# Performance work log

Measured on AMD Instinct MI355X. Metric: run time of the kernel, lower is better.

The kernel has to match this reference:

```python
import jax, jax.numpy as jnp
import numpy as np

N_NODES = 10000
N_EDGES = 640000
IN_FEATS = 128
HIDDEN = 128
N_CLASSES = 64
EPS = 0.0


def _linear_params(key, fan_in, fan_out):
    k1, k2 = jax.random.split(key)
    bound = 1.0 / np.sqrt(fan_in)
    W = jax.random.uniform(k1, (fan_in, fan_out), jnp.float32, -bound, bound)
    b = jax.random.uniform(k2, (fan_out,), jnp.float32, -bound, bound)
    return W, b


def setup_inputs() -> dict:
    key = jax.random.key(0)
    ks = jax.random.split(key, 8)
    features = jax.random.normal(ks[0], (N_NODES, IN_FEATS), jnp.float32)
    src = jax.random.randint(ks[1], (N_EDGES,), 0, N_NODES, jnp.int64 if jax.config.jax_enable_x64 else jnp.int32)
    dst = jax.random.randint(ks[2], (N_EDGES,), 0, N_NODES, jnp.int64 if jax.config.jax_enable_x64 else jnp.int32)
    W1, b1 = _linear_params(ks[3], IN_FEATS, HIDDEN)
    W3, b3 = _linear_params(ks[4], HIDDEN, HIDDEN)
    W4, b4 = _linear_params(ks[5], HIDDEN, HIDDEN)
    W2, b2 = _linear_params(ks[6], HIDDEN, N_CLASSES)
    return {"features": features, "src": src, "dst": dst,
            "W1": W1, "b1": b1, "W3": W3, "b3": b3,
            "W4": W4, "b4": b4, "W2": W2, "b2": b2}


def gin_conv(h, src, dst, W, b):
    # sum-aggregate neighbor features: agg[v] = sum_{(u->v)} h[u]
    agg = jax.ops.segment_sum(h[src], dst, num_segments=N_NODES)
    z = (1.0 + EPS) * h + agg
    return z @ W + b


def reference(features, src, dst, W1, b1, W3, b3, W4, b4, W2, b2):
    h = gin_conv(features, src, dst, W1, b1)
    h = jax.nn.relu(h)
    h = gin_conv(h, src, dst, W3, b3)
    h = jax.nn.relu(h)
    h = gin_conv(h, src, dst, W4, b4)
    h = jax.nn.relu(h)
    h = gin_conv(h, src, dst, W2, b2)
    return h
```

## Files before the change

kernel.cpp:

```cpp
#include <hip/hip_runtime.h>
#include <hip/hip_bf16.h>

#define N_NODES 10000
#define N_EDGES 640000
#define FEATS   128
#define CAP     192
#define NBUCK   157
#define ECHUNK  2048
#define NPB     313
#define OSTR    160
#define TILE    8

typedef __attribute__((ext_vector_type(2))) float f32x2;

__device__ __forceinline__ float bflo(uint p) { return __uint_as_float(p << 16); }
__device__ __forceinline__ float bfhi(uint p) { return __uint_as_float(p & 0xffff0000u); }
__device__ __forceinline__ f32x2 unpk(uint p) {
    f32x2 v;
    v.x = __uint_as_float(p << 16);
    v.y = __uint_as_float(p & 0xffff0000u);
    return v;
}


__global__ __launch_bounds__(256) void bin_pack(const int* __restrict__ src,
                                                const int* __restrict__ dst,
                                                uint* __restrict__ bucketed,
                                                ushort* __restrict__ goffs,
                                                const float* __restrict__ features,
                                                ushort* __restrict__ hb0) {
    __shared__ int hist[NBUCK];
    __shared__ int offs[NBUCK + 1];
    __shared__ int scan[256];
    __shared__ uint staging[ECHUNK];
    const int tid = threadIdx.x;
    const int b = blockIdx.x;
    const int e0 = b * ECHUNK;
    for (int i = tid; i < NBUCK; i += 256) hist[i] = 0;
    __syncthreads();
    int dreg[8];
#pragma unroll
    for (int i = 0; i < 8; ++i) {
        int e = e0 + tid + i * 256;
        dreg[i] = (e < N_EDGES) ? dst[e] : -1;
        if (dreg[i] >= 0) atomicAdd(&hist[dreg[i] >> 6], 1);
    }
    __syncthreads();
    int val = (tid < NBUCK) ? hist[tid] : 0;
    scan[tid] = val;
    __syncthreads();
    for (int off = 1; off < 256; off <<= 1) {
        int t = (tid >= off) ? scan[tid - off] : 0;
        __syncthreads();
        scan[tid] += t;
        __syncthreads();
    }
    if (tid < NBUCK) offs[tid] = scan[tid] - val;
    if (tid == 0) offs[NBUCK] = scan[NBUCK - 1];
    for (int i = tid; i < NBUCK; i += 256) hist[i] = 0;
    __syncthreads();
    if (tid <= NBUCK) goffs[b * OSTR + tid] = (ushort)offs[tid];
#pragma unroll
    for (int i = 0; i < 8; ++i) {
        int e = e0 + tid + i * 256;
        if (dreg[i] >= 0) {
            int s = src[e];
            int bk = dreg[i] >> 6;
            int slot = offs[bk] + atomicAdd(&hist[bk], 1);
            staging[slot] = ((uint)s << 6) | (uint)(dreg[i] & 63);
        }
    }
    __syncthreads();
    uint4* gu = (uint4*)(bucketed + (size_t)b * ECHUNK);
    const uint4* lu = (const uint4*)staging;
#pragma unroll
    for (int i = 0; i < ECHUNK / 4 / 256; ++i)
        gu[tid + i * 256] = lu[tid + i * 256];

    const int n4 = N_NODES * FEATS / 4;
    for (int i = b * 256 + tid; i < n4; i += NPB * 256) {
        float4 f = ((const float4*)features)[i];
        __hip_bfloat16 b0 = __float2bfloat16(f.x);
        __hip_bfloat16 b1 = __float2bfloat16(f.y);
        __hip_bfloat16 b2 = __float2bfloat16(f.z);
        __hip_bfloat16 b3 = __float2bfloat16(f.w);
        ushort4 o;
        o.x = *(const ushort*)&b0; o.y = *(const ushort*)&b1;
        o.z = *(const ushort*)&b2; o.w = *(const ushort*)&b3;
        ((ushort4*)hb0)[i] = o;
    }
}


__global__ __launch_bounds__(256) void build_ell(const uint* __restrict__ bucketed,
                                                 const ushort* __restrict__ goffs,
                                                 ushort* __restrict__ ell,
                                                 int* __restrict__ cnts) {
    __shared__ ushort lell[64 * CAP];
    __shared__ int lcur[64];
    const int tid = threadIdx.x;
    const int bk = blockIdx.x;
    if (tid < 64) lcur[tid] = 0;
    __syncthreads();
    for (int b = tid; b < NPB; b += 256) {
        int off0 = goffs[b * OSTR + bk];
        int off1 = goffs[b * OSTR + bk + 1];
        const uint* p0 = bucketed + (size_t)b * ECHUNK;
        for (int i = off0; i < off1; ++i) {
            uint p = p0[i];
            int v = p & 63;
            int slot = atomicAdd(&lcur[v], 1);
            if (slot < CAP) lell[v * CAP + slot] = (ushort)(p >> 6);
        }
    }
    __syncthreads();
    const int node0 = bk * 64;
    int nn = N_NODES - node0;
    if (nn > 64) nn = 64;
    const uint4* lu = (const uint4*)lell;
    uint4* gu = (uint4*)(ell + (size_t)node0 * CAP);
    const int nq = nn * (CAP / 8);
    for (int i = tid; i < nq; i += 256) gu[i] = lu[i];
    for (int v = tid; v < nn; v += 256) {
        int c = lcur[v];
        cnts[node0 + v] = (c > CAP) ? CAP : c;
    }
}


__device__ __forceinline__ void gather_tile(const uint4* __restrict__ hbq,
                                            const int* __restrict__ cnts,
                                            const ushort* __restrict__ ell,
                                            int tile0, int tid,
                                            float (*sZ)[132]) {
    const int lane = tid & 63;
    const int wv = tid >> 6;
    const int g = lane >> 4;
    const int q = lane & 15;
#pragma unroll
    for (int n = 0; n < 2; ++n) {
        const int v = tile0 + wv * 2 + n;
        int cnt = cnts[v];
        if (cnt > CAP) cnt = CAP;
        const ushort* __restrict__ row = ell + (size_t)v * CAP;
        f32x2 acc[4];
#pragma unroll
        for (int i = 0; i < 4; ++i) acc[i] = (f32x2){0.f, 0.f};
        const int jmain = cnt & ~3;
#pragma unroll 2
        for (int j = 0; j < jmain; j += 4) {
            uint2 iv = *(const uint2*)(row + j);
            uint word = (g & 2) ? iv.y : iv.x;
            uint u = (g & 1) ? (word >> 16) : (word & 0xffffu);
            uint4 p = hbq[u * 16 + q];
            acc[0] += unpk(p.x);
            acc[1] += unpk(p.y);
            acc[2] += unpk(p.z);
            acc[3] += unpk(p.w);
        }
        if (jmain < cnt) {
            uint2 iv = *(const uint2*)(row + jmain);
            uint word = (g & 2) ? iv.y : iv.x;
            uint u = (g & 1) ? (word >> 16) : (word & 0xffffu);
            float scale = (jmain + g < cnt) ? 1.0f : 0.0f;
            if (u > N_NODES - 1) u = N_NODES - 1;
            f32x2 s2 = {scale, scale};
            uint4 p = hbq[u * 16 + q];
            acc[0] += unpk(p.x) * s2;
            acc[1] += unpk(p.y) * s2;
            acc[2] += unpk(p.z) * s2;
            acc[3] += unpk(p.w) * s2;
        }
        float a[8] = {acc[0].x, acc[0].y, acc[1].x, acc[1].y,
                      acc[2].x, acc[2].y, acc[3].x, acc[3].y};
#pragma unroll
        for (int d = 16; d < 64; d <<= 1) {
#pragma unroll
            for (int i = 0; i < 8; ++i) a[i] += __shfl_xor(a[i], d);
        }
        if (g == 0) {
            uint4 p = hbq[(size_t)v * 16 + q];
            a[0] += bflo(p.x); a[1] += bfhi(p.x);
            a[2] += bflo(p.y); a[3] += bfhi(p.y);
            a[4] += bflo(p.z); a[5] += bfhi(p.z);
            a[6] += bflo(p.w); a[7] += bfhi(p.w);
            float4 a0 = {a[0], a[1], a[2], a[3]};
            float4 a1 = {a[4], a[5], a[6], a[7]};
            *(float4*)&sZ[wv * 2 + n][q * 8]     = a0;
            *(float4*)&sZ[wv * 2 + n][q * 8 + 4] = a1;
        }
    }
}


__global__ __launch_bounds__(256) void fused_kernel(const ushort* __restrict__ hb,
                                                    const float* __restrict__ W,
                                                    const float* __restrict__ bias,
                                                    const int* __restrict__ cnts,
                                                    const ushort* __restrict__ ell,
                                                    ushort* __restrict__ hb_out) {
    __shared__ float sZ[TILE][132];
    const int tile0 = blockIdx.x * TILE;
    const int tid = threadIdx.x;
    gather_tile((const uint4*)hb, cnts, ell, tile0, tid, sZ);
    __syncthreads();

    const int col = tid & 127;
    const int gg  = tid >> 7;
    float acc2[4] = {0.f, 0.f, 0.f, 0.f};
#pragma unroll 2
    for (int k = 0; k < 128; k += 4) {
        float w0 = W[(k + 0) * 128 + col];
        float w1 = W[(k + 1) * 128 + col];
        float w2 = W[(k + 2) * 128 + col];
        float w3 = W[(k + 3) * 128 + col];
#pragma unroll
        for (int r = 0; r < 4; ++r) {
            float4 z = *(const float4*)&sZ[gg * 4 + r][k];
            acc2[r] = fmaf(z.x, w0, acc2[r]);
            acc2[r] = fmaf(z.y, w1, acc2[r]);
            acc2[r] = fmaf(z.z, w2, acc2[r]);
            acc2[r] = fmaf(z.w, w3, acc2[r]);
        }
    }
    const float b = bias[col];
#pragma unroll
    for (int r = 0; r < 4; ++r) {
        const int vv = tile0 + gg * 4 + r;
        float y = fmaxf(acc2[r] + b, 0.f);
        __hip_bfloat16 bv = __float2bfloat16(y);
        hb_out[(size_t)vv * FEATS + col] = *(const ushort*)&bv;
    }
}


__global__ __launch_bounds__(256) void fused3_kernel(const ushort* __restrict__ hb,
                                                     const float* __restrict__ W4,
                                                     const float* __restrict__ b4,
                                                     const float* __restrict__ W2,
                                                     const int* __restrict__ cnts,
                                                     const ushort* __restrict__ ell,
                                                     ushort* __restrict__ yb64) {
    __shared__ float sZ[TILE][132];
    __shared__ float sH[TILE][132];
    const int tile0 = blockIdx.x * TILE;
    const int tid = threadIdx.x;
    gather_tile((const uint4*)hb, cnts, ell, tile0, tid, sZ);
    __syncthreads();

    {
        const int col = tid & 127;
        const int gg  = tid >> 7;
        float acc2[4] = {0.f, 0.f, 0.f, 0.f};
#pragma unroll 2
        for (int k = 0; k < 128; k += 4) {
            float w0 = W4[(k + 0) * 128 + col];
            float w1 = W4[(k + 1) * 128 + col];
            float w2 = W4[(k + 2) * 128 + col];
            float w3 = W4[(k + 3) * 128 + col];
#pragma unroll
            for (int r = 0; r < 4; ++r) {
                float4 z = *(const float4*)&sZ[gg * 4 + r][k];
                acc2[r] = fmaf(z.x, w0, acc2[r]);
                acc2[r] = fmaf(z.y, w1, acc2[r]);
                acc2[r] = fmaf(z.z, w2, acc2[r]);
                acc2[r] = fmaf(z.w, w3, acc2[r]);
            }
        }
        const float b = b4[col];
#pragma unroll
        for (int r = 0; r < 4; ++r)
            sH[gg * 4 + r][col] = fmaxf(acc2[r] + b, 0.f);
    }
    __syncthreads();

    {
        const int col = tid & 63;
        const int gg  = tid >> 6;
        float acc3[2] = {0.f, 0.f};
#pragma unroll 2
        for (int k = 0; k < 128; k += 4) {
            float w0 = W2[(k + 0) * 64 + col];
            float w1 = W2[(k + 1) * 64 + col];
            float w2 = W2[(k + 2) * 64 + col];
            float w3 = W2[(k + 3) * 64 + col];
#pragma unroll
            for (int r = 0; r < 2; ++r) {
                float4 z = *(const float4*)&sH[gg * 2 + r][k];
                acc3[r] = fmaf(z.x, w0, acc3[r]);
                acc3[r] = fmaf(z.y, w1, acc3[r]);
                acc3[r] = fmaf(z.z, w2, acc3[r]);
                acc3[r] = fmaf(z.w, w3, acc3[r]);
            }
        }
#pragma unroll
        for (int r = 0; r < 2; ++r) {
            const int vv = tile0 + gg * 2 + r;
            __hip_bfloat16 bv = __float2bfloat16(acc3[r]);
            yb64[(size_t)vv * 64 + col] = *(const ushort*)&bv;
        }
    }
}


__global__ __launch_bounds__(256) void agg64(const ushort* __restrict__ yb,
                                             const int* __restrict__ cnts,
                                             const ushort* __restrict__ ell,
                                             const float* __restrict__ bias,
                                             float* __restrict__ out) {
    const int v = blockIdx.x * 4 + (threadIdx.x >> 6);
    const int lane = threadIdx.x & 63;
    const int g = lane >> 3;
    const int q = lane & 7;
    int cnt = cnts[v];
    if (cnt > CAP) cnt = CAP;
    const ushort* __restrict__ row = ell + (size_t)v * CAP;
    const uint4* __restrict__ ybq = (const uint4*)yb;
    f32x2 acc[4];
#pragma unroll
    for (int i = 0; i < 4; ++i) acc[i] = (f32x2){0.f, 0.f};
    const int jmain = cnt & ~7;
#pragma unroll 2
    for (int j = 0; j < jmain; j += 8) {
        uint4 iv = *(const uint4*)(row + j);
        uint a = (g & 2) ? iv.y : iv.x;
        uint b = (g & 2) ? iv.w : iv.z;
        uint word = (g & 4) ? b : a;
        uint u = (g & 1) ? (word >> 16) : (word & 0xffffu);
        uint4 p = ybq[u * 8 + q];
        acc[0] += unpk(p.x);
        acc[1] += unpk(p.y);
        acc[2] += unpk(p.z);
        acc[3] += unpk(p.w);
    }
    if (jmain < cnt) {
        uint4 iv = *(const uint4*)(row + jmain);
        uint a = (g & 2) ? iv.y : iv.x;
        uint b = (g & 2) ? iv.w : iv.z;
        uint word = (g & 4) ? b : a;
        uint u = (g & 1) ? (word >> 16) : (word & 0xffffu);
        float scale = (jmain + g < cnt) ? 1.0f : 0.0f;
        if (u > N_NODES - 1) u = N_NODES - 1;
        f32x2 s2 = {scale, scale};
        uint4 p = ybq[u * 8 + q];
        acc[0] += unpk(p.x) * s2;
        acc[1] += unpk(p.y) * s2;
        acc[2] += unpk(p.z) * s2;
        acc[3] += unpk(p.w) * s2;
    }
    float a[8] = {acc[0].x, acc[0].y, acc[1].x, acc[1].y,
                  acc[2].x, acc[2].y, acc[3].x, acc[3].y};
#pragma unroll
    for (int d = 8; d < 64; d <<= 1) {
#pragma unroll
        for (int i = 0; i < 8; ++i) a[i] += __shfl_xor(a[i], d);
    }
    if (g == 0) {
        uint4 p = ybq[(size_t)v * 8 + q];
        const float4* br = (const float4*)bias;
        float4 b0 = br[q * 2], b1 = br[q * 2 + 1];
        float4 o0, o1;
        o0.x = a[0] + bflo(p.x) + b0.x; o0.y = a[1] + bfhi(p.x) + b0.y;
        o0.z = a[2] + bflo(p.y) + b0.z; o0.w = a[3] + bfhi(p.y) + b0.w;
        o1.x = a[4] + bflo(p.z) + b1.x; o1.y = a[5] + bfhi(p.z) + b1.y;
        o1.z = a[6] + bflo(p.w) + b1.z; o1.w = a[7] + bfhi(p.w) + b1.w;
        float4* outr = (float4*)(out + (size_t)v * 64);
        outr[q * 2]     = o0;
        outr[q * 2 + 1] = o1;
    }
}


extern "C" void kernel_launch(void* const* d_in, const int* in_sizes, int n_in,
                              void* d_out, int out_size, void* d_ws, size_t ws_size,
                              hipStream_t stream) {
    const float* features = (const float*)d_in[0];
    const int*   src      = (const int*)d_in[1];
    const int*   dst      = (const int*)d_in[2];
    const float* W1 = (const float*)d_in[3];
    const float* b1 = (const float*)d_in[4];
    const float* W3 = (const float*)d_in[5];
    const float* b3 = (const float*)d_in[6];
    const float* W4 = (const float*)d_in[7];
    const float* b4 = (const float*)d_in[8];
    const float* W2 = (const float*)d_in[9];
    const float* b2 = (const float*)d_in[10];
    float* out = (float*)d_out;

    int*    cnts     = (int*)d_ws;
    ushort* goffs    = (ushort*)(cnts + 10240);
    uint*   bucketed = (uint*)(goffs + 50240);
    ushort* ell      = (ushort*)(bucketed + (size_t)NPB * ECHUNK);
    ushort* hb0      = ell + (size_t)N_NODES * CAP;
    ushort* hb1      = hb0 + (size_t)N_NODES * FEATS;
    ushort* yb64     = hb1 + (size_t)N_NODES * FEATS;

    bin_pack<<<NPB, 256, 0, stream>>>(src, dst, bucketed, goffs, features, hb0);
    build_ell<<<NBUCK, 256, 0, stream>>>(bucketed, goffs, ell, cnts);

    const int fblocks = N_NODES / TILE;

    fused_kernel<<<fblocks, 256, 0, stream>>>(hb0, W1, b1, cnts, ell, hb1);
    fused_kernel<<<fblocks, 256, 0, stream>>>(hb1, W3, b3, cnts, ell, hb0);
    fused3_kernel<<<fblocks, 256, 0, stream>>>(hb0, W4, b4, W2, cnts, ell, yb64);
    agg64<<<N_NODES / 4, 256, 0, stream>>>(yb64, cnts, ell, b2, out);
}
```

Before: 114.7 us.

## Sort nodes by degree for balanced tiles and use packed bf16 weights

Adds a degree histogram, a scan and a scatter that build a permutation of nodes sorted by neighbour count. The fused gather+matmul kernels then process nodes in that order, so each tile holds nodes of similar degree and wavefronts sit idle less. The weights are also pre-converted to packed bf16 pairs and the matmuls use two-wide float math. This adds two small kernels and an extra indirection, and bf16 weights lose some precision.

```diff
diff --git a/kernel.cpp b/kernel.cpp
--- a/kernel.cpp
+++ b/kernel.cpp
@@ -21,6 +21,10 @@
     v.y = __uint_as_float(p & 0xffff0000u);
     return v;
 }
+__device__ __forceinline__ uint pk2(float a, float b) {
+    __hip_bfloat16 x = __float2bfloat16(a), y = __float2bfloat16(b);
+    return (uint)(*(const ushort*)&x) | ((uint)(*(const ushort*)&y) << 16);
+}
 
 
 __global__ __launch_bounds__(256) void bin_pack(const int* __restrict__ src,
@@ -28,7 +32,16 @@
                                                 uint* __restrict__ bucketed,
                                                 ushort* __restrict__ goffs,
                                                 const float* __restrict__ features,
-                                                ushort* __restrict__ hb0) {
+                                                ushort* __restrict__ hb0,
+                                                const float* __restrict__ W1,
+                                                const float* __restrict__ W3,
+                                                const float* __restrict__ W4,
+                                                const float* __restrict__ W2,
+                                                uint* __restrict__ w1p,
+                                                uint* __restrict__ w3p,
+                                                uint* __restrict__ w4p,
+                                                uint* __restrict__ w2p,
+                                                int* __restrict__ bins) {
     __shared__ int hist[NBUCK];
     __shared__ int offs[NBUCK + 1];
     __shared__ int scan[256];
@@ -36,6 +49,7 @@
     const int tid = threadIdx.x;
     const int b = blockIdx.x;
     const int e0 = b * ECHUNK;
+    if (b == 0) bins[tid] = 0;
     for (int i = tid; i < NBUCK; i += 256) hist[i] = 0;
     __syncthreads();
     int dreg[8];
@@ -77,25 +91,25 @@
     for (int i = 0; i < ECHUNK / 4 / 256; ++i)
         gu[tid + i * 256] = lu[tid + i * 256];
 
+    const int gid = b * 256 + tid;
+    const int GSZ = NPB * 256;
     const int n4 = N_NODES * FEATS / 4;
-    for (int i = b * 256 + tid; i < n4; i += NPB * 256) {
+    for (int i = gid; i < n4; i += GSZ) {
         float4 f = ((const float4*)features)[i];
-        __hip_bfloat16 b0 = __float2bfloat16(f.x);
-        __hip_bfloat16 b1 = __float2bfloat16(f.y);
-        __hip_bfloat16 b2 = __float2bfloat16(f.z);
-        __hip_bfloat16 b3 = __float2bfloat16(f.w);
-        ushort4 o;
-        o.x = *(const ushort*)&b0; o.y = *(const ushort*)&b1;
-        o.z = *(const ushort*)&b2; o.w = *(const ushort*)&b3;
-        ((ushort4*)hb0)[i] = o;
-    }
+        ((uint2*)hb0)[i] = (uint2){pk2(f.x, f.y), pk2(f.z, f.w)};
+    }
+    for (int i = gid; i < 128 * 64; i += GSZ) w1p[i] = pk2(W1[2 * i], W1[2 * i + 1]);
+    for (int i = gid; i < 128 * 64; i += GSZ) w3p[i] = pk2(W3[2 * i], W3[2 * i + 1]);
+    for (int i = gid; i < 128 * 64; i += GSZ) w4p[i] = pk2(W4[2 * i], W4[2 * i + 1]);
+    for (int i = gid; i < 128 * 32; i += GSZ) w2p[i] = pk2(W2[2 * i], W2[2 * i + 1]);
 }
 
 
 __global__ __launch_bounds__(256) void build_ell(const uint* __restrict__ bucketed,
                                                  const ushort* __restrict__ goffs,
                                                  ushort* __restrict__ ell,
-                                                 int* __restrict__ cnts) {
+                                                 int* __restrict__ cnts,
+                                                 int* __restrict__ bins) {
     __shared__ ushort lell[64 * CAP];
     __shared__ int lcur[64];
     const int tid = threadIdx.x;
@@ -123,14 +137,43 @@
     for (int i = tid; i < nq; i += 256) gu[i] = lu[i];
     for (int v = tid; v < nn; v += 256) {
         int c = lcur[v];
-        cnts[node0 + v] = (c > CAP) ? CAP : c;
-    }
+        c = (c > CAP) ? CAP : c;
+        cnts[node0 + v] = c;
+        atomicAdd(&bins[c], 1);
+    }
+}
+
+
+__global__ __launch_bounds__(256) void scan256(const int* __restrict__ bins,
+                                               int* __restrict__ binofs) {
+    __shared__ int s[256];
+    const int t = threadIdx.x;
+    int v = bins[t];
+    s[t] = v;
+    __syncthreads();
+    for (int off = 1; off < 256; off <<= 1) {
+        int u = (t >= off) ? s[t - off] : 0;
+        __syncthreads();
+        s[t] += u;
+        __syncthreads();
+    }
+    binofs[t] = s[t] - v;
+}
+
+__global__ __launch_bounds__(256) void scatter_perm(const int* __restrict__ cnts,
+                                                    int* __restrict__ binofs,
+                                                    ushort* __restrict__ perm) {
+    int v = blockIdx.x * 256 + threadIdx.x;
+    if (v >= N_NODES) return;
+    int slot = atomicAdd(&binofs[cnts[v]], 1);
+    perm[slot] = (ushort)v;
 }
 
 
 __device__ __forceinline__ void gather_tile(const uint4* __restrict__ hbq,
                                             const int* __restrict__ cnts,
                                             const ushort* __restrict__ ell,
+                                            const ushort* __restrict__ perm,
                                             int tile0, int tid,
                                             float (*sZ)[132]) {
     const int lane = tid & 63;
@@ -139,7 +182,7 @@
     const int q = lane & 15;
 #pragma unroll
     for (int n = 0; n < 2; ++n) {
-        const int v = tile0 + wv * 2 + n;
+        const int v = perm[tile0 + wv * 2 + n];
         int cnt = cnts[v];
         if (cnt > CAP) cnt = CAP;
         const ushort* __restrict__ row = ell + (size_t)v * CAP;
@@ -194,111 +237,100 @@
 
 
 __global__ __launch_bounds__(256) void fused_kernel(const ushort* __restrict__ hb,
-                                                    const float* __restrict__ W,
+                                                    const uint* __restrict__ Wb,
                                                     const float* __restrict__ bias,
                                                     const int* __restrict__ cnts,
                                                     const ushort* __restrict__ ell,
+                                                    const ushort* __restrict__ perm,
                                                     ushort* __restrict__ hb_out) {
     __shared__ float sZ[TILE][132];
     const int tile0 = blockIdx.x * TILE;
     const int tid = threadIdx.x;
-    gather_tile((const uint4*)hb, cnts, ell, tile0, tid, sZ);
-    __syncthreads();
-
-    const int col = tid & 127;
-    const int gg  = tid >> 7;
-    float acc2[4] = {0.f, 0.f, 0.f, 0.f};
+    gather_tile((const uint4*)hb, cnts, ell, perm, tile0, tid, sZ);
+    __syncthreads();
+
+    const int cp = tid & 63;
+    const int gg = tid >> 6;
+    f32x2 acc2[2] = {{0.f, 0.f}, {0.f, 0.f}};
 #pragma unroll 2
-    for (int k = 0; k < 128; k += 4) {
-        float w0 = W[(k + 0) * 128 + col];
-        float w1 = W[(k + 1) * 128 + col];
-        float w2 = W[(k + 2) * 128 + col];
-        float w3 = W[(k + 3) * 128 + col];
-#pragma unroll
-        for (int r = 0; r < 4; ++r) {
-            float4 z = *(const float4*)&sZ[gg * 4 + r][k];
-            acc2[r] = fmaf(z.x, w0, acc2[r]);
-            acc2[r] = fmaf(z.y, w1, acc2[r]);
-            acc2[r] = fmaf(z.z, w2, acc2[r]);
-            acc2[r] = fmaf(z.w, w3, acc2[r]);
-        }
-    }
-    const float b = bias[col];
-#pragma unroll
-    for (int r = 0; r < 4; ++r) {
-        const int vv = tile0 + gg * 4 + r;
-        float y = fmaxf(acc2[r] + b, 0.f);
-        __hip_bfloat16 bv = __float2bfloat16(y);
-        hb_out[(size_t)vv * FEATS + col] = *(const ushort*)&bv;
+    for (int k = 0; k < 128; k += 2) {
+        f32x2 w0 = unpk(Wb[(k + 0) * 64 + cp]);
+        f32x2 w1 = unpk(Wb[(k + 1) * 64 + cp]);
+#pragma unroll
+        for (int r = 0; r < 2; ++r) {
+            float z0 = sZ[gg * 2 + r][k];
+            float z1 = sZ[gg * 2 + r][k + 1];
+            acc2[r] += w0 * z0;
+            acc2[r] += w1 * z1;
+        }
+    }
+    float2 bb = ((const float2*)bias)[cp];
+    uint* outp = (uint*)hb_out;
+#pragma unroll
+    for (int r = 0; r < 2; ++r) {
+        const int vv = perm[tile0 + gg * 2 + r];
+        float y0 = fmaxf(acc2[r].x + bb.x, 0.f);
+        float y1 = fmaxf(acc2[r].y + bb.y, 0.f);
+        outp[(size_t)vv * 64 + cp] = pk2(y0, y1);
     }
 }
 
 
 __global__ __launch_bounds__(256) void fused3_kernel(const ushort* __restrict__ hb,
-                                                     const float* __restrict__ W4,
+                                                     const uint* __restrict__ W4b,
                                                      const float* __restrict__ b4,
-                                                     const float* __restrict__ W2,
+                                                     const uint* __restrict__ W2b,
                                                      const int* __restrict__ cnts,
                                                      const ushort* __restrict__ ell,
+                                                     const ushort* __restrict__ perm,
                                                      ushort* __restrict__ yb64) {
     __shared__ float sZ[TILE][132];
     __shared__ float sH[TILE][132];
     const int tile0 = blockIdx.x * TILE;
     const int tid = threadIdx.x;
-    gather_tile((const uint4*)hb, cnts, ell, tile0, tid, sZ);
+    gather_tile((const uint4*)hb, cnts, ell, perm, tile0, tid, sZ);
     __syncthreads();
 
     {
-        const int col = tid & 127;
-        const int gg  = tid >> 7;
-        float acc2[4] = {0.f, 0.f, 0.f, 0.f};
+        const int cp = tid & 63;
+        const int gg = tid >> 6;
+        f32x2 acc2[2] = {{0.f, 0.f}, {0.f, 0.f}};
 #pragma unroll 2
-        for (int k = 0; k < 128; k += 4) {
-            float w0 = W4[(k + 0) * 128 + col];
-            float w1 = W4[(k + 1) * 128 + col];
-            float w2 = W4[(k + 2) * 128 + col];
-            float w3 = W4[(k + 3) * 128 + col];
-#pragma unroll
-            for (int r = 0; r < 4; ++r) {
-                float4 z = *(const float4*)&sZ[gg * 4 + r][k];
-                acc2[r] = fmaf(z.x, w0, acc2[r]);
-                acc2[r] = fmaf(z.y, w1, acc2[r]);
-                acc2[r] = fmaf(z.z, w2, acc2[r]);
-                acc2[r] = fmaf(z.w, w3, acc2[r]);
+        for (int k = 0; k < 128; k += 2) {
+            f32x2 w0 = unpk(W4b[(k + 0) * 64 + cp]);
+            f32x2 w1 = unpk(W4b[(k + 1) * 64 + cp]);
+#pragma unroll
+            for (int r = 0; r < 2; ++r) {
+                float z0 = sZ[gg * 2 + r][k];
+                float z1 = sZ[gg * 2 + r][k + 1];
+                acc2[r] += w0 * z0;
+                acc2[r] += w1 * z1;
             }
         }
-        const float b = b4[col];
-#pragma unroll
-        for (int r = 0; r < 4; ++r)
-            sH[gg * 4 + r][col] = fmaxf(acc2[r] + b, 0.f);
+        float2 bb = ((const float2*)b4)[cp];
+#pragma unroll
+        for (int r = 0; r < 2; ++r) {
+            sH[gg * 2 + r][cp * 2]     = fmaxf(acc2[r].x + bb.x, 0.f);
+            sH[gg * 2 + r][cp * 2 + 1] = fmaxf(acc2[r].y + bb.y, 0.f);
+        }
     }
     __syncthreads();
 
     {
-        const int col = tid & 63;
-        const int gg  = tid >> 6;
-        float acc3[2] = {0.f, 0.f};
+        const int cp = tid & 31;
+        const int gg = tid >> 5;
+        f32x2 acc3 = {0.f, 0.f};
 #pragma unroll 2
-        for (int k = 0; k < 128; k += 4) {
-            float w0 = W2[(k + 0) * 64 + col];
-            float w1 = W2[(k + 1) * 64 + col];
-            float w2 = W2[(k + 2) * 64 + col];
-            float w3 = W2[(k + 3) * 64 + col];
-#pragma unroll
-            for (int r = 0; r < 2; ++r) {
-                float4 z = *(const float4*)&sH[gg * 2 + r][k];
-                acc3[r] = fmaf(z.x, w0, acc3[r]);
-                acc3[r] = fmaf(z.y, w1, acc3[r]);
-                acc3[r] = fmaf(z.z, w2, acc3[r]);
-                acc3[r] = fmaf(z.w, w3, acc3[r]);
-            }
-        }
-#pragma unroll
-        for (int r = 0; r < 2; ++r) {
-            const int vv = tile0 + gg * 2 + r;
-            __hip_bfloat16 bv = __float2bfloat16(acc3[r]);
-            yb64[(size_t)vv * 64 + col] = *(const ushort*)&bv;
-        }
+        for (int k = 0; k < 128; k += 2) {
+            f32x2 w0 = unpk(W2b[(k + 0) * 32 + cp]);
+            f32x2 w1 = unpk(W2b[(k + 1) * 32 + cp]);
+            float z0 = sH[gg][k];
+            float z1 = sH[gg][k + 1];
+            acc3 += w0 * z0;
+            acc3 += w1 * z1;
+        }
+        const int vv = perm[tile0 + gg];
+        ((uint*)yb64)[(size_t)vv * 32 + cp] = pk2(acc3.x, acc3.y);
     }
 }
 
@@ -388,20 +420,30 @@
     float* out = (float*)d_out;
 
     int*    cnts     = (int*)d_ws;
-    ushort* goffs    = (ushort*)(cnts + 10240);
+    int*    bins     = cnts + 10240;
+    int*    binofs   = bins + 256;
+    ushort* perm     = (ushort*)(binofs + 256);
+    ushort* goffs    = perm + 10240;
     uint*   bucketed = (uint*)(goffs + 50240);
     ushort* ell      = (ushort*)(bucketed + (size_t)NPB * ECHUNK);
     ushort* hb0      = ell + (size_t)N_NODES * CAP;
     ushort* hb1      = hb0 + (size_t)N_NODES * FEATS;
     ushort* yb64     = hb1 + (size_t)N_NODES * FEATS;
-
-    bin_pack<<<NPB, 256, 0, stream>>>(src, dst, bucketed, goffs, features, hb0);
-    build_ell<<<NBUCK, 256, 0, stream>>>(bucketed, goffs, ell, cnts);
+    uint*   w1p      = (uint*)(yb64 + (size_t)N_NODES * 64);
+    uint*   w3p      = w1p + 128 * 64;
+    uint*   w4p      = w3p + 128 * 64;
+    uint*   w2p      = w4p + 128 * 64;
+
+    bin_pack<<<NPB, 256, 0, stream>>>(src, dst, bucketed, goffs, features, hb0,
+                                      W1, W3, W4, W2, w1p, w3p, w4p, w2p, bins);
+    build_ell<<<NBUCK, 256, 0, stream>>>(bucketed, goffs, ell, cnts, bins);
+    scan256<<<1, 256, 0, stream>>>(bins, binofs);
+    scatter_perm<<<40, 256, 0, stream>>>(cnts, binofs, perm);
 
     const int fblocks = N_NODES / TILE;
 
-    fused_kernel<<<fblocks, 256, 0, stream>>>(hb0, W1, b1, cnts, ell, hb1);
-    fused_kernel<<<fblocks, 256, 0, stream>>>(hb1, W3, b3, cnts, ell, hb0);
-    fused3_kernel<<<fblocks, 256, 0, stream>>>(hb0, W4, b4, W2, cnts, ell, yb64);
+    fused_kernel<<<fblocks, 256, 0, stream>>>(hb0, w1p, b1, cnts, ell, perm, hb1);
+    fused_kernel<<<fblocks, 256, 0, stream>>>(hb1, w3p, b3, cnts, ell, perm, hb0);
+    fused3_kernel<<<fblocks, 256, 0, stream>>>(hb0, w4p, b4, w2p, cnts, ell, perm, yb64);
     agg64<<<N_NODES / 4, 256, 0, stream>>>(yb64, cnts, ell, b2, out);
 }
```

Measured after the change: 155.9 us. 1.36x slower.
